# Optimization experiments

Hardware: AMD Instinct MI355X
Metric: run time of the kernel (lower is better)

## Reference

```python
import jax, jax.numpy as jnp
import numpy as np


def _kan_layer(comb, W1, b1, W2, b2, Wc, bc):
    # comb: [B, D]; W1,b1,W2: [D, K]; b2: [D]; Wc: [D, H]; bc: [H]
    # per-feature MLP: Linear(1,K) -> ReLU -> Linear(K,1), batched over D
    h = jax.nn.relu(comb[:, :, None] * W1[None, :, :] + b1[None, :, :])  # [B, D, K]
    u = jnp.einsum('bdk,dk->bd', h, W2) + b2[None, :]                    # [B, D]
    return u @ Wc + bc[None, :]                                          # [B, H]


def setup_inputs() -> dict:
    key = jax.random.key(0)
    ks = jax.random.split(key, 9)
    B, I, H, K = 2048, 256, 512, 32
    D = I + H
    s = 0.05
    return {
        'x': jax.random.normal(ks[0], (B, I), dtype=jnp.float32),
        'h_prev': jax.random.normal(ks[1], (B, H), dtype=jnp.float32),
        'c_prev': jax.random.normal(ks[2], (B, H), dtype=jnp.float32),
        'W1': jax.random.normal(ks[3], (4, D, K), dtype=jnp.float32) * s,
        'b1': jax.random.normal(ks[4], (4, D, K), dtype=jnp.float32) * s,
        'W2': jax.random.normal(ks[5], (4, D, K), dtype=jnp.float32) * s,
        'b2': jax.random.normal(ks[6], (4, D), dtype=jnp.float32) * s,
        'Wc': jax.random.normal(ks[7], (4, D, H), dtype=jnp.float32) * s,
        'bc': jax.random.normal(ks[8], (4, H), dtype=jnp.float32) * s,
    }


def reference(x, h_prev, c_prev, W1, b1, W2, b2, Wc, bc):
    comb = jnp.concatenate([x, h_prev], axis=1)  # [B, D]
    # gate order: 0=forget, 1=input, 2=output, 3=cell
    gates = [_kan_layer(comb, W1[g], b1[g], W2[g], b2[g], Wc[g], bc[g])
             for g in range(4)]
    f_t = jax.nn.sigmoid(gates[0])
    i_t = jax.nn.sigmoid(gates[1])
    o_t = jax.nn.sigmoid(gates[2])
    c_tilde = jnp.tanh(gates[3])
    c_t = f_t * c_prev + i_t * c_tilde
    h_t = o_t * jnp.tanh(c_t)
    return (h_t, c_t)
```

## Files before the change

kernel.cpp:

```cpp
#include <hip/hip_runtime.h>

#define B_  2048
#define I_  256
#define H_  512
#define D_  768
#define K_  32

typedef unsigned short ushort_t;
typedef unsigned int uint_t;
typedef __attribute__((ext_vector_type(8))) __bf16 bf16x8;
typedef __attribute__((ext_vector_type(4))) float f32x4;

__device__ __forceinline__ ushort_t f2bf(float f) {
  uint_t u = __float_as_uint(f);
  u += 0x7fffu + ((u >> 16) & 1u);
  return (ushort_t)(u >> 16);
}
__device__ __forceinline__ float fast_sigmoid(float x) {
  return 1.f / (1.f + __expf(-x));
}
__device__ __forceinline__ float fast_tanh(float x) {
  float t = __expf(2.f * fabsf(x));
  float r = 1.f - 2.f / (t + 1.f);
  return copysignf(r, x);
}
__device__ __forceinline__ void gload16(const void* g, void* l) {
  __builtin_amdgcn_global_load_lds(
      (const __attribute__((address_space(1))) void*)g,
      (__attribute__((address_space(3))) void*)l, 16, 0, 0);
}

__global__ __launch_bounds__(256) void transpose_all(
    const float* __restrict__ W1, const float* __restrict__ b1,
    const float* __restrict__ W2, const float* __restrict__ Wc,
    float* __restrict__ w1t, float* __restrict__ b1t, float* __restrict__ w2t,
    ushort_t* __restrict__ wcT) {
  __shared__ float t[32][33];
  int tx = threadIdx.x & 31, ty = threadIdx.x >> 5;
  int bid = blockIdx.x;
  if (bid < 288) {
    int z = bid / 96;
    int g = (bid / 24) % 4;
    int d0 = (bid % 24) * 32;
    const float* src = (z == 0) ? W1 : (z == 1) ? b1 : W2;
    float* dst       = (z == 0) ? w1t : (z == 1) ? b1t : w2t;
#pragma unroll
    for (int i = 0; i < 4; ++i) {
      int r = ty + i * 8;
      t[r][tx] = src[((size_t)g * D_ + d0 + r) * K_ + tx];
    }
    __syncthreads();
#pragma unroll
    for (int i = 0; i < 4; ++i) {
      int r = ty + i * 8;
      dst[((size_t)g * K_ + r) * D_ + d0 + tx] = t[tx][r];
    }
  } else {
    int r2 = bid - 288;
    int g = r2 / 384;
    int rem = r2 % 384;
    int d0 = (rem / 16) * 32;
    int h0 = (rem % 16) * 32;
#pragma unroll
    for (int i = 0; i < 4; ++i) {
      int r = ty + i * 8;
      t[r][tx] = Wc[((size_t)g * D_ + d0 + r) * H_ + h0 + tx];
    }
    __syncthreads();
#pragma unroll
    for (int i = 0; i < 4; ++i) {
      int r = ty + i * 8;
      wcT[((size_t)g * H_ + h0 + r) * D_ + d0 + tx] = f2bf(t[tx][r]);
    }
  }
}

__global__ __launch_bounds__(256) void kan_phase1(
    const float* __restrict__ x, const float* __restrict__ hp,
    const float* __restrict__ w1t, const float* __restrict__ b1t,
    const float* __restrict__ w2t, const float* __restrict__ b2,
    ushort_t* __restrict__ uT) {
  int bi = blockIdx.x;
  int g = bi & 3;
  int rest = bi >> 2;
  int dc = rest % 3;
  int bc = rest / 3;
  int t = threadIdx.x;
  int d = dc * 256 + t;

  float w1[K_], bb[K_], w2[K_];
#pragma unroll
  for (int k = 0; k < K_; ++k) {
    w1[k] = w1t[((size_t)g * K_ + k) * D_ + d];
    bb[k] = b1t[((size_t)g * K_ + k) * D_ + d];
    w2[k] = w2t[((size_t)g * K_ + k) * D_ + d];
  }
  float bias = b2[(size_t)g * D_ + d];

  const float* src = (dc == 0) ? (x + t) : (hp + ((dc == 1) ? t : t + 256));
  int stride = (dc == 0) ? I_ : H_;
  int b0 = bc * 32;

#pragma unroll
  for (int bb8 = 0; bb8 < 32; bb8 += 8) {
    float cv[8], acc[8];
#pragma unroll
    for (int j = 0; j < 8; ++j) {
      cv[j] = src[(size_t)(b0 + bb8 + j) * stride];
      acc[j] = bias;
    }
#pragma unroll
    for (int k = 0; k < K_; ++k) {
#pragma unroll
      for (int j = 0; j < 8; ++j) {
        float h = fmaxf(fmaf(cv[j], w1[k], bb[k]), 0.f);
        acc[j] = fmaf(h, w2[k], acc[j]);
      }
    }
#pragma unroll
    for (int j = 0; j < 8; ++j)
      uT[((size_t)g * B_ + b0 + bb8 + j) * D_ + d] = f2bf(acc[j]);
  }
}

#define TB 32
#define TH 64
#define BK 32
#define NT (D_ / BK)
#define BUFSZ 24576
#define NBUF 3

__global__ __launch_bounds__(512, 4) void kan_phase2(
    const ushort_t* __restrict__ uT, const ushort_t* __restrict__ wcT,
    const float* __restrict__ bc, const float* __restrict__ cprev,
    float* __restrict__ out) {
  __shared__ __align__(16) char smem[NBUF * BUFSZ];
  const int b0 = blockIdx.x * TB;
  const int h0 = blockIdx.y * TH;
  const int t = threadIdx.x;
  const int w = t >> 6;
  const int l = t & 63;

  const int ag   = w >> 1;
  const int arow = (w & 1) * 16 + (l >> 2);
  const int acg  = (l & 3) ^ ((arow ^ (arow >> 2)) & 3);
  const ushort_t* asrc = uT + ((size_t)ag * B_ + b0 + arow) * D_ + acg * 8;
  const int bg0  = w >> 2;
  const int brow = (w & 3) * 16 + (l >> 2);
  const int bcg  = (l & 3) ^ ((brow ^ (brow >> 2)) & 3);
  const ushort_t* bsrc0 = wcT + ((size_t)bg0 * H_ + h0 + brow) * D_ + bcg * 8;
  const ushort_t* bsrc1 = bsrc0 + (size_t)2 * H_ * D_;
  const int aoffL  = (w << 10) + (l << 4);
  const int boff0L = 8192 + (w << 10) + (l << 4);
  const int boff1L = 8192 + ((w + 8) << 10) + (l << 4);

  const int gate = w >> 1, nh = w & 1;
  const int frow = l & 15, c0 = l >> 4;
  const int cx = ((c0 ^ ((frow ^ (frow >> 2)) & 3)) << 4);
  int aoff[2], boff[2];
#pragma unroll
  for (int m = 0; m < 2; ++m)
    aoff[m] = ((gate * 32 + m * 16 + frow) << 6) + cx;
#pragma unroll
  for (int n = 0; n < 2; ++n)
    boff[n] = 8192 + ((gate * 64 + nh * 32 + n * 16 + frow) << 6) + cx;

  f32x4 acc[2][2];
#pragma unroll
  for (int n = 0; n < 2; ++n) {
    float bv = bc[(size_t)gate * H_ + h0 + nh * 32 + n * 16 + frow];
#pragma unroll
    for (int m = 0; m < 2; ++m) acc[m][n] = (f32x4){bv, bv, bv, bv};
  }

  auto stage = [&](int bufoff, int dke) {
    gload16(asrc + dke, smem + bufoff + aoffL);
    gload16(bsrc0 + dke, smem + bufoff + boff0L);
    gload16(bsrc1 + dke, smem + bufoff + boff1L);
  };
  auto compute = [&](const char* bb) {
    bf16x8 af0 = *(const bf16x8*)(bb + aoff[0]);
    bf16x8 af1 = *(const bf16x8*)(bb + aoff[1]);
    bf16x8 bf0 = *(const bf16x8*)(bb + boff[0]);
    bf16x8 bf1 = *(const bf16x8*)(bb + boff[1]);
    acc[0][0] = __builtin_amdgcn_mfma_f32_16x16x32_bf16(af0, bf0, acc[0][0], 0, 0, 0);
    acc[0][1] = __builtin_amdgcn_mfma_f32_16x16x32_bf16(af0, bf1, acc[0][1], 0, 0, 0);
    acc[1][0] = __builtin_amdgcn_mfma_f32_16x16x32_bf16(af1, bf0, acc[1][0], 0, 0, 0);
    acc[1][1] = __builtin_amdgcn_mfma_f32_16x16x32_bf16(af1, bf1, acc[1][1], 0, 0, 0);
  };

  stage(0, 0);
  stage(BUFSZ, BK);
  int roff = 0, soff = 2 * BUFSZ;
  for (int s = 0; s < NT - 1; ++s) {
    asm volatile("s_waitcnt vmcnt(3)" ::: "memory");
    __builtin_amdgcn_s_barrier();
    if (s + 2 < NT) {
      stage(soff, (s + 2) * BK);
      soff += BUFSZ; if (soff == NBUF * BUFSZ) soff = 0;
    }
    compute(smem + roff);
    roff += BUFSZ; if (roff == NBUF * BUFSZ) roff = 0;
  }
  asm volatile("s_waitcnt vmcnt(0)" ::: "memory");
  __builtin_amdgcn_s_barrier();
  compute(smem + roff);
  __syncthreads();

  float* gf = (float*)smem;
#pragma unroll
  for (int m = 0; m < 2; ++m)
#pragma unroll
    for (int n = 0; n < 2; ++n)
#pragma unroll
      for (int e = 0; e < 4; ++e) {
        int row = m * 16 + (l >> 4) * 4 + e;
        int col = nh * 32 + n * 16 + frow;
        gf[((size_t)gate * 32 + row) * 68 + col] = acc[m][n][e];
      }
  __syncthreads();

  {
    int row = t >> 4;
    int ch = t & 15;
    int b = b0 + row;
    int hc = h0 + ch * 4;
    f32x4 g0 = *(const f32x4*)&gf[((size_t)0 * 32 + row) * 68 + ch * 4];
    f32x4 g1 = *(const f32x4*)&gf[((size_t)1 * 32 + row) * 68 + ch * 4];
    f32x4 g2 = *(const f32x4*)&gf[((size_t)2 * 32 + row) * 68 + ch * 4];
    f32x4 g3 = *(const f32x4*)&gf[((size_t)3 * 32 + row) * 68 + ch * 4];
    f32x4 cp = *(const f32x4*)&cprev[(size_t)b * H_ + hc];
    f32x4 hv, cv;
#pragma unroll
    for (int e = 0; e < 4; ++e) {
      float ft = fast_sigmoid(g0[e]);
      float it = fast_sigmoid(g1[e]);
      float ot = fast_sigmoid(g2[e]);
      float tc = fast_tanh(g3[e]);
      float cn = ft * cp[e] + it * tc;
      cv[e] = cn;
      hv[e] = ot * fast_tanh(cn);
    }
    *(f32x4*)&out[(size_t)b * H_ + hc] = hv;
    *(f32x4*)&out[(size_t)B_ * H_ + (size_t)b * H_ + hc] = cv;
  }
}

extern "C" void kernel_launch(void* const* d_in, const int* in_sizes, int n_in,
                              void* d_out, int out_size, void* d_ws, size_t ws_size,
                              hipStream_t stream) {
  const float* x  = (const float*)d_in[0];
  const float* hp = (const float*)d_in[1];
  const float* cp = (const float*)d_in[2];
  const float* W1 = (const float*)d_in[3];
  const float* b1 = (const float*)d_in[4];
  const float* W2 = (const float*)d_in[5];
  const float* b2 = (const float*)d_in[6];
  const float* Wc = (const float*)d_in[7];
  const float* bc = (const float*)d_in[8];
  float* out = (float*)d_out;

  float* w1t = (float*)d_ws;
  float* b1t = w1t + 98304;
  float* w2t = b1t + 98304;
  ushort_t* wcT = (ushort_t*)(w2t + 98304);
  ushort_t* uT  = wcT + (size_t)4 * H_ * D_;

  transpose_all<<<1824, 256, 0, stream>>>(W1, b1, W2, Wc, w1t, b1t, w2t, wcT);
  kan_phase1<<<768, 256, 0, stream>>>(x, hp, w1t, b1t, w2t, b2, uT);
  kan_phase2<<<dim3(B_ / TB, H_ / TH), 512, 0, stream>>>(uT, wcT, bc, cp, out);
}
```

Before: 50.80 us.

## Fuse weight transpose and per-feature MLP into one prep kernel, swizzle phase2 blocks

Merges the Wc transpose/bf16 conversion and the per-feature MLP phase into a single launch. The MLP blocks now read W1/b1/W2 directly with float4 loads instead of going through pre-transposed copies, which removes one kernel launch and one round trip through workspace. The GEMM kernel switches to a flattened, swizzled block index to improve L2 reuse, and raises wave priority around the MFMA sequence. Reading the weights per thread as strided float4 rows is less coalesced than the transposed layout, so the fused kernel may run slower than the old MLP phase.

```diff
diff --git a/kernel.cpp b/kernel.cpp
--- a/kernel.cpp
+++ b/kernel.cpp
@@ -30,96 +30,79 @@
       (__attribute__((address_space(3))) void*)l, 16, 0, 0);
 }
 
-__global__ __launch_bounds__(256) void transpose_all(
+__global__ __launch_bounds__(256) void kan_prep(
+    const float* __restrict__ x, const float* __restrict__ hp,
     const float* __restrict__ W1, const float* __restrict__ b1,
-    const float* __restrict__ W2, const float* __restrict__ Wc,
-    float* __restrict__ w1t, float* __restrict__ b1t, float* __restrict__ w2t,
-    ushort_t* __restrict__ wcT) {
-  __shared__ float t[32][33];
-  int tx = threadIdx.x & 31, ty = threadIdx.x >> 5;
+    const float* __restrict__ W2, const float* __restrict__ b2,
+    const float* __restrict__ Wc,
+    ushort_t* __restrict__ wcT, ushort_t* __restrict__ uT) {
+  __shared__ float ttile[32][33];
   int bid = blockIdx.x;
-  if (bid < 288) {
-    int z = bid / 96;
-    int g = (bid / 24) % 4;
-    int d0 = (bid % 24) * 32;
-    const float* src = (z == 0) ? W1 : (z == 1) ? b1 : W2;
-    float* dst       = (z == 0) ? w1t : (z == 1) ? b1t : w2t;
+  if (bid < 1536) {
+    int tx = threadIdx.x & 31, ty = threadIdx.x >> 5;
+    int g = bid / 384;
+    int rem = bid % 384;
+    int d0 = (rem / 16) * 32;
+    int h0 = (rem % 16) * 32;
 #pragma unroll
     for (int i = 0; i < 4; ++i) {
       int r = ty + i * 8;
-      t[r][tx] = src[((size_t)g * D_ + d0 + r) * K_ + tx];
+      ttile[r][tx] = Wc[((size_t)g * D_ + d0 + r) * H_ + h0 + tx];
     }
     __syncthreads();
 #pragma unroll
     for (int i = 0; i < 4; ++i) {
       int r = ty + i * 8;
-      dst[((size_t)g * K_ + r) * D_ + d0 + tx] = t[tx][r];
+      wcT[((size_t)g * H_ + h0 + r) * D_ + d0 + tx] = f2bf(ttile[tx][r]);
     }
   } else {
-    int r2 = bid - 288;
-    int g = r2 / 384;
-    int rem = r2 % 384;
-    int d0 = (rem / 16) * 32;
-    int h0 = (rem % 16) * 32;
-#pragma unroll
-    for (int i = 0; i < 4; ++i) {
-      int r = ty + i * 8;
-      t[r][tx] = Wc[((size_t)g * D_ + d0 + r) * H_ + h0 + tx];
-    }
-    __syncthreads();
-#pragma unroll
-    for (int i = 0; i < 4; ++i) {
-      int r = ty + i * 8;
-      wcT[((size_t)g * H_ + h0 + r) * D_ + d0 + tx] = f2bf(t[tx][r]);
-    }
-  }
-}
-
-__global__ __launch_bounds__(256) void kan_phase1(
-    const float* __restrict__ x, const float* __restrict__ hp,
-    const float* __restrict__ w1t, const float* __restrict__ b1t,
-    const float* __restrict__ w2t, const float* __restrict__ b2,
-    ushort_t* __restrict__ uT) {
-  int bi = blockIdx.x;
-  int g = bi & 3;
-  int rest = bi >> 2;
-  int dc = rest % 3;
-  int bc = rest / 3;
-  int t = threadIdx.x;
-  int d = dc * 256 + t;
-
-  float w1[K_], bb[K_], w2[K_];
-#pragma unroll
-  for (int k = 0; k < K_; ++k) {
-    w1[k] = w1t[((size_t)g * K_ + k) * D_ + d];
-    bb[k] = b1t[((size_t)g * K_ + k) * D_ + d];
-    w2[k] = w2t[((size_t)g * K_ + k) * D_ + d];
-  }
-  float bias = b2[(size_t)g * D_ + d];
-
-  const float* src = (dc == 0) ? (x + t) : (hp + ((dc == 1) ? t : t + 256));
-  int stride = (dc == 0) ? I_ : H_;
-  int b0 = bc * 32;
-
-#pragma unroll
-  for (int bb8 = 0; bb8 < 32; bb8 += 8) {
-    float cv[8], acc[8];
-#pragma unroll
-    for (int j = 0; j < 8; ++j) {
-      cv[j] = src[(size_t)(b0 + bb8 + j) * stride];
-      acc[j] = bias;
-    }
-#pragma unroll
-    for (int k = 0; k < K_; ++k) {
+    int p = bid - 1536;
+    int combo = p >> 6;
+    int bc = p & 63;
+    int g = combo & 3;
+    int dc = combo >> 2;
+    int t = threadIdx.x;
+    int d = dc * 256 + t;
+
+    f32x4 w1v[8], bbv[8], w2v[8];
+    const float* W1p = W1 + ((size_t)g * D_ + d) * K_;
+    const float* b1p = b1 + ((size_t)g * D_ + d) * K_;
+    const float* W2p = W2 + ((size_t)g * D_ + d) * K_;
+#pragma unroll
+    for (int q = 0; q < 8; ++q) {
+      w1v[q] = *(const f32x4*)(W1p + q * 4);
+      bbv[q] = *(const f32x4*)(b1p + q * 4);
+      w2v[q] = *(const f32x4*)(W2p + q * 4);
+    }
+    float bias = b2[(size_t)g * D_ + d];
+
+    const float* src = (dc == 0) ? (x + t) : (hp + ((dc == 1) ? t : t + 256));
+    int stride = (dc == 0) ? I_ : H_;
+    int b0 = bc * 32;
+
+#pragma unroll
+    for (int bb8 = 0; bb8 < 32; bb8 += 8) {
+      float cv[8], acc[8];
 #pragma unroll
       for (int j = 0; j < 8; ++j) {
-        float h = fmaxf(fmaf(cv[j], w1[k], bb[k]), 0.f);
-        acc[j] = fmaf(h, w2[k], acc[j]);
+        cv[j] = src[(size_t)(b0 + bb8 + j) * stride];
+        acc[j] = bias;
       }
-    }
-#pragma unroll
-    for (int j = 0; j < 8; ++j)
-      uT[((size_t)g * B_ + b0 + bb8 + j) * D_ + d] = f2bf(acc[j]);
+#pragma unroll
+      for (int q = 0; q < 8; ++q)
+#pragma unroll
+        for (int e = 0; e < 4; ++e) {
+          float w1 = w1v[q][e], bbk = bbv[q][e], w2 = w2v[q][e];
+#pragma unroll
+          for (int j = 0; j < 8; ++j) {
+            float h = fmaxf(fmaf(cv[j], w1, bbk), 0.f);
+            acc[j] = fmaf(h, w2, acc[j]);
+          }
+        }
+#pragma unroll
+      for (int j = 0; j < 8; ++j)
+        uT[((size_t)g * B_ + b0 + bb8 + j) * D_ + d] = f2bf(acc[j]);
+    }
   }
 }
 
@@ -135,8 +118,11 @@
     const float* __restrict__ bc, const float* __restrict__ cprev,
     float* __restrict__ out) {
   __shared__ __align__(16) char smem[NBUF * BUFSZ];
-  const int b0 = blockIdx.x * TB;
-  const int h0 = blockIdx.y * TH;
+  const int flat = blockIdx.x;
+  const int bxx = ((flat & 7) << 3) | ((flat >> 3) & 7);
+  const int byy = flat >> 6;
+  const int b0 = bxx * TB;
+  const int h0 = byy * TH;
   const int t = threadIdx.x;
   const int w = t >> 6;
   const int l = t & 63;
@@ -183,10 +169,12 @@
     bf16x8 af1 = *(const bf16x8*)(bb + aoff[1]);
     bf16x8 bf0 = *(const bf16x8*)(bb + boff[0]);
     bf16x8 bf1 = *(const bf16x8*)(bb + boff[1]);
+    __builtin_amdgcn_s_setprio(1);
     acc[0][0] = __builtin_amdgcn_mfma_f32_16x16x32_bf16(af0, bf0, acc[0][0], 0, 0, 0);
     acc[0][1] = __builtin_amdgcn_mfma_f32_16x16x32_bf16(af0, bf1, acc[0][1], 0, 0, 0);
     acc[1][0] = __builtin_amdgcn_mfma_f32_16x16x32_bf16(af1, bf0, acc[1][0], 0, 0, 0);
     acc[1][1] = __builtin_amdgcn_mfma_f32_16x16x32_bf16(af1, bf1, acc[1][1], 0, 0, 0);
+    __builtin_amdgcn_s_setprio(0);
   };
 
   stage(0, 0);
@@ -260,13 +248,9 @@
   const float* bc = (const float*)d_in[8];
   float* out = (float*)d_out;
 
-  float* w1t = (float*)d_ws;
-  float* b1t = w1t + 98304;
-  float* w2t = b1t + 98304;
-  ushort_t* wcT = (ushort_t*)(w2t + 98304);
+  ushort_t* wcT = (ushort_t*)d_ws;
   ushort_t* uT  = wcT + (size_t)4 * H_ * D_;
 
-  transpose_all<<<1824, 256, 0, stream>>>(W1, b1, W2, Wc, w1t, b1t, w2t, wcT);
-  kan_phase1<<<768, 256, 0, stream>>>(x, hp, w1t, b1t, w2t, b2, uT);
-  kan_phase2<<<dim3(B_ / TB, H_ / TH), 512, 0, stream>>>(uT, wcT, bc, cp, out);
-}
+  kan_prep<<<2304, 256, 0, stream>>>(x, hp, W1, b1, W2, b2, Wc, wcT, uT);
+  kan_phase2<<<(B_ / TB) * (H_ / TH), 512, 0, stream>>>(uT, wcT, bc, cp, out);
+}
```

Result: no change. 51.55 us (+1.5%).
